# Performance work log

Measured on AMD Instinct MI355X. Metric: run time of the kernel, lower is better.

The kernel has to match this reference:

```python
import jax, jax.numpy as jnp
import numpy as np


def setup_inputs() -> dict:
    key = jax.random.key(0)
    k_x, k_w1, k_w2 = jax.random.split(key, 3)
    B, N, F, H = 32, 1024, 512, 2048
    x = jax.random.normal(k_x, (B, N, F), dtype=jnp.float32)
    # first: orthogonal-ish init (Gaussian is fine as a stand-in for correctness testing)
    W1 = jax.random.normal(k_w1, (H, F), dtype=jnp.float32) / np.sqrt(F)
    b1 = jnp.zeros((H,), dtype=jnp.float32)
    # second: normal(std=0.01)
    W2 = jax.random.normal(k_w2, (F, H), dtype=jnp.float32) * 0.01
    b2 = jnp.zeros((F,), dtype=jnp.float32)
    return {"x": x, "W1": W1, "b1": b1, "W2": W2, "b2": b2, "dim": 1}


def reference(x, W1, b1, W2, b2, dim):
    # Move the target feature axis (1 + dim) to last position.
    x = jnp.moveaxis(x, 1 + dim, -1)  # [B, N, F]
    srt = jnp.argsort(x, axis=-1)     # argsort indices
    inv = jnp.argsort(srt, axis=-1)   # inverse permutation
    # torch: x.scatter(-1, argsort, x) -> out[argsort[i]] = x[i] == gather by inverse
    xs = jnp.take_along_axis(x, inv, axis=-1)
    # 2-layer MLP with skip
    h = jax.nn.relu(jnp.einsum('bnf,hf->bnh', xs, W1) + b1)
    y = jnp.einsum('bnh,fh->bnf', h, W2) + b2 + xs
    # torch: y.scatter(-1, inverse, y) -> out[inverse[i]] = y[i] == gather by argsort
    out = jnp.take_along_axis(y, srt, axis=-1)
    return jnp.moveaxis(out, -1, 1 + dim)
```

## Files before the change

### kernel.cpp

```cpp
#include <hip/hip_runtime.h>
#include <hip/hip_bf16.h>

typedef __hip_bfloat16 bf16;
typedef __attribute__((ext_vector_type(8))) short bf16x8;
typedef __attribute__((ext_vector_type(4))) float f32x4;

#define ASYNC_CP16(gsrc, ldst)                                                              \
  __builtin_amdgcn_global_load_lds(                                                         \
      (const __attribute__((address_space(1))) unsigned int*)(gsrc),                        \
      (__attribute__((address_space(3))) unsigned int*)(ldst), 16, 0, 0)

#define BB 32
#define NN 1024
#define FF 512
#define HH 2048
#define M_ROWS (BB * NN)

__global__ __launch_bounds__(256) void cvt_pair(const float* __restrict__ a, bf16* __restrict__ da,
                                                const float* __restrict__ b, bf16* __restrict__ db,
                                                int n) {
  int i = blockIdx.x * 256 + threadIdx.x;
  if (i < n) {
    da[i] = __float2bfloat16(a[i]);
    db[i] = __float2bfloat16(b[i]);
  }
}

template <int CTRL>
__device__ __forceinline__ unsigned long long dpp_xor64(unsigned long long k) {
  int lo = (int)(unsigned)k;
  int hi = (int)(unsigned)(k >> 32);
  int plo = __builtin_amdgcn_update_dpp(lo, lo, CTRL, 0xF, 0xF, false);
  int phi = __builtin_amdgcn_update_dpp(hi, hi, CTRL, 0xF, 0xF, false);
  return (((unsigned long long)(unsigned)phi) << 32) | (unsigned)plo;
}

__global__ __launch_bounds__(256) void sort_rows_wave(const float* __restrict__ x,
                                                      unsigned* __restrict__ xs_pack,
                                                      unsigned* __restrict__ srt_pack) {
  __shared__ __align__(16) unsigned short scatx[4 * FF];
  const int t = threadIdx.x;
  const int lane = t & 63;
  const int w = t >> 6;
  const size_t row = (size_t)blockIdx.x * 4 + w;
  const float* xr = x + row * FF;

  float4 v0 = *(const float4*)(xr + lane * 8);
  float4 v1 = *(const float4*)(xr + lane * 8 + 4);
  float vals[8] = {v0.x, v0.y, v0.z, v0.w, v1.x, v1.y, v1.z, v1.w};

  unsigned long long key[8];
#pragma unroll
  for (int r = 0; r < 8; r++) {
    unsigned u = __float_as_uint(vals[r]);
    unsigned s = u ^ ((unsigned)((int)u >> 31) | 0x80000000u);
    key[r] = ((unsigned long long)s << 32) | (unsigned)(lane * 8 + r);
  }

#pragma unroll
  for (int k = 2; k <= 512; k <<= 1) {
#pragma unroll
    for (int j = k >> 1; j > 0; j >>= 1) {
      if (j >= 8) {
        const int d = j >> 3;
#pragma unroll
        for (int r = 0; r < 8; r++) {
          unsigned long long o;
          if (d == 1)       o = dpp_xor64<0xB1>(key[r]);
          else if (d == 2)  o = dpp_xor64<0x4E>(key[r]);
          else if (d == 8)  o = dpp_xor64<0x128>(key[r]);
          else              o = __shfl_xor(key[r], d, 64);
          bool asc = (((lane * 8 + r) & k) == 0);
          bool lower = ((lane & d) == 0);
          bool keepmin = (asc == lower);
          bool minemin = key[r] < o;
          key[r] = (minemin == keepmin) ? key[r] : o;
        }
      } else {
#pragma unroll
        for (int r = 0; r < 8; r++) {
          if ((r & j) == 0) {
            const int a = r, b = r | j;
            bool asc = (((lane * 8 + a) & k) == 0);
            unsigned long long ka = key[a], kb = key[b];
            bool sw = ((ka > kb) == asc);
            key[a] = sw ? kb : ka;
            key[b] = sw ? ka : kb;
          }
        }
      }
    }
  }

  const int base = w * FF;
  unsigned j8[8];
#pragma unroll
  for (int r = 0; r < 8; r++) {
    j8[r] = (unsigned)key[r] & 0xFFFFu;
    __hip_bfloat16 hb = __float2bfloat16(vals[r]);
    scatx[base + j8[r]] = *(unsigned short*)&hb;
  }

  uint4 so;
  so.x = j8[0] | (j8[1] << 16);
  so.y = j8[2] | (j8[3] << 16);
  so.z = j8[4] | (j8[5] << 16);
  so.w = j8[6] | (j8[7] << 16);
  *(uint4*)(srt_pack + row * 256 + lane * 4) = so;

  __syncthreads();
  uint4 xo = *(const uint4*)&scatx[base + lane * 8];
  *(uint4*)(xs_pack + row * 256 + lane * 4) = xo;
}

template <int RELU, int ADDX, int K, int N>
__global__ __launch_bounds__(512, 4) void gemm_fat(const bf16* __restrict__ A,
                                                   const bf16* __restrict__ Bw,
                                                   const float* __restrict__ bias,
                                                   const bf16* __restrict__ xs_add,
                                                   bf16* __restrict__ C) {
  __shared__ __align__(16) bf16 As[128 * 32];
  __shared__ __align__(16) bf16 Bs[256 * 32];
  const int t = threadIdx.x;
  const int lane = t & 63, wave = t >> 6;
  const int waveM = wave >> 2, waveN = wave & 3;
  const int srow = lane >> 2;
  const int scol = (lane & 3) * 8;
  const size_t mBase = (size_t)blockIdx.x * 128;
  const size_t nBase = (size_t)blockIdx.y * 256;
  const bf16* Ag  = A  + (mBase + wave * 16 + srow) * (size_t)K + scol;
  const bf16* Bg0 = Bw + (nBase + wave * 32 + srow) * (size_t)K + scol;
  const bf16* Bg1 = Bw + (nBase + wave * 32 + 16 + srow) * (size_t)K + scol;
  bf16* Al  = &As[wave * 16 * 32];
  bf16* Bl0 = &Bs[wave * 32 * 32];
  bf16* Bl1 = &Bs[(wave * 32 + 16) * 32];
  const int fr = lane & 15;
  const int fk = (lane >> 4) * 8;

  f32x4 acc[4][4];
  f32x4 zero = {0.f, 0.f, 0.f, 0.f};
#pragma unroll
  for (int i = 0; i < 4; i++)
#pragma unroll
    for (int j = 0; j < 4; j++) acc[i][j] = zero;

  for (int k0 = 0; k0 < K; k0 += 32) {
    ASYNC_CP16(Ag + k0, Al);
    ASYNC_CP16(Bg0 + k0, Bl0);
    ASYNC_CP16(Bg1 + k0, Bl1);
    __syncthreads();
    bf16x8 af[4], bfr[4];
#pragma unroll
    for (int mt = 0; mt < 4; mt++)
      af[mt] = *(const bf16x8*)&As[(waveM * 64 + mt * 16 + fr) * 32 + fk];
#pragma unroll
    for (int nt = 0; nt < 4; nt++)
      bfr[nt] = *(const bf16x8*)&Bs[(waveN * 64 + nt * 16 + fr) * 32 + fk];
#pragma unroll
    for (int mt = 0; mt < 4; mt++)
#pragma unroll
      for (int nt = 0; nt < 4; nt++)
        acc[mt][nt] = __builtin_amdgcn_mfma_f32_16x16x32_bf16(af[mt], bfr[nt], acc[mt][nt], 0, 0, 0);
    __syncthreads();
  }

  const int cn = lane & 15;
  const int cm = (lane >> 4) * 4;
  float b4[4];
#pragma unroll
  for (int nt = 0; nt < 4; nt++) b4[nt] = bias[nBase + waveN * 64 + nt * 16 + cn];
#pragma unroll
  for (int mt = 0; mt < 4; mt++) {
#pragma unroll
    for (int nt = 0; nt < 4; nt++) {
      size_t gn = nBase + waveN * 64 + nt * 16 + cn;
#pragma unroll
      for (int r = 0; r < 4; r++) {
        size_t gm = mBase + waveM * 64 + mt * 16 + cm + r;
        float v = acc[mt][nt][r] + b4[nt];
        if (RELU) v = fmaxf(v, 0.f);
        if (ADDX) v += __bfloat162float(xs_add[gm * N + gn]);
        C[gm * N + gn] = __float2bfloat16(v);
      }
    }
  }
}

__global__ __launch_bounds__(256) void permute_gather(const bf16* __restrict__ zp,
                                                      const unsigned* __restrict__ srt_pack,
                                                      float* __restrict__ out) {
  __shared__ __align__(16) unsigned short zr[4][FF];
  const int t = threadIdx.x;
  const int lane = t & 63;
  const int w = t >> 6;
  const size_t row = (size_t)blockIdx.x * 4 + w;

  *(uint4*)&zr[w][lane * 8] = *(const uint4*)(zp + row * FF + lane * 8);
  uint4 sv = *(const uint4*)(srt_pack + row * 256 + lane * 4);
  __syncthreads();

  unsigned idx[8] = {sv.x & 0xFFFFu, sv.x >> 16, sv.y & 0xFFFFu, sv.y >> 16,
                     sv.z & 0xFFFFu, sv.z >> 16, sv.w & 0xFFFFu, sv.w >> 16};
  float4 o0, o1;
#pragma unroll
  for (int r = 0; r < 8; r++) {
    float zf = __uint_as_float(((unsigned)zr[w][idx[r]]) << 16);
    ((r < 4) ? (&o0.x) : (&o1.x))[r & 3] = zf;
  }
  *(float4*)(out + row * FF + lane * 8) = o0;
  *(float4*)(out + row * FF + lane * 8 + 4) = o1;
}

extern "C" void kernel_launch(void* const* d_in, const int* in_sizes, int n_in,
                              void* d_out, int out_size, void* d_ws, size_t ws_size,
                              hipStream_t stream) {
  const float* x  = (const float*)d_in[0];
  const float* W1 = (const float*)d_in[1];
  const float* b1 = (const float*)d_in[2];
  const float* W2 = (const float*)d_in[3];
  const float* b2 = (const float*)d_in[4];
  float* out = (float*)d_out;

  char* ws = (char*)d_ws;
  unsigned* xs  = (unsigned*)(ws);
  bf16*     xsb = (bf16*)(ws);
  bf16*     z   = (bf16*)(ws);
  unsigned* srt = (unsigned*)(ws + 33554432);
  bf16* h   = (bf16*)(ws + 67108864);
  bf16* W1b = (bf16*)(ws + 201326592);
  bf16* W2b = (bf16*)(ws + 203423744);

  cvt_pair<<<(HH * FF + 255) / 256, 256, 0, stream>>>(W1, W1b, W2, W2b, HH * FF);
  sort_rows_wave<<<M_ROWS / 4, 256, 0, stream>>>(x, xs, srt);
  gemm_fat<1, 0, FF, HH><<<dim3(M_ROWS / 128, HH / 256), 512, 0, stream>>>(xsb, W1b, b1, nullptr, h);
  gemm_fat<0, 1, HH, FF><<<dim3(M_ROWS / 128, FF / 256), 512, 0, stream>>>(h, W2b, b2, xsb, z);
  permute_gather<<<M_ROWS / 4, 256, 0, stream>>>(z, srt, out);
}
```

Baseline: 376.0 us.

## Rewrite GEMM with 256x256 tiles, double-buffered LDS prefetch and swizzled layout

Replaces the single-buffered 128x256 GEMM with a 256x256 tile kernel. It stages the next 64-wide K slice into a second LDS buffer while MFMAs run on the current one, using XOR-swizzled LDS addressing to avoid bank conflicts. It also adds explicit waitcnt/barrier scheduling and setprio around the MFMA bursts. This aims to hide global-load latency and raise arithmetic intensity, at the cost of 128KB of LDS, 2 blocks per CU and more accumulator registers.

```diff
diff --git a/kernel.cpp b/kernel.cpp
--- a/kernel.cpp
+++ b/kernel.cpp
@@ -114,73 +114,161 @@
 }
 
 template <int RELU, int ADDX, int K, int N>
-__global__ __launch_bounds__(512, 4) void gemm_fat(const bf16* __restrict__ A,
-                                                   const bf16* __restrict__ Bw,
-                                                   const float* __restrict__ bias,
-                                                   const bf16* __restrict__ xs_add,
-                                                   bf16* __restrict__ C) {
-  __shared__ __align__(16) bf16 As[128 * 32];
-  __shared__ __align__(16) bf16 Bs[256 * 32];
+__global__ __launch_bounds__(512, 2) void gemm8p(const bf16* __restrict__ A,
+                                                 const bf16* __restrict__ Bw,
+                                                 const float* __restrict__ bias,
+                                                 const bf16* __restrict__ xs_add,
+                                                 bf16* __restrict__ C) {
+  __shared__ __align__(16) bf16 S[65536];
   const int t = threadIdx.x;
   const int lane = t & 63, wave = t >> 6;
   const int waveM = wave >> 2, waveN = wave & 3;
-  const int srow = lane >> 2;
-  const int scol = (lane & 3) * 8;
-  const size_t mBase = (size_t)blockIdx.x * 128;
+  const size_t mBase = (size_t)blockIdx.x * 256;
   const size_t nBase = (size_t)blockIdx.y * 256;
-  const bf16* Ag  = A  + (mBase + wave * 16 + srow) * (size_t)K + scol;
-  const bf16* Bg0 = Bw + (nBase + wave * 32 + srow) * (size_t)K + scol;
-  const bf16* Bg1 = Bw + (nBase + wave * 32 + 16 + srow) * (size_t)K + scol;
-  bf16* Al  = &As[wave * 16 * 32];
-  bf16* Bl0 = &Bs[wave * 32 * 32];
-  bf16* Bl1 = &Bs[(wave * 32 + 16) * 32];
+
+  const int srow = t >> 2;
+  const int sclog = (t & 3) ^ ((t >> 3) & 3);
+  const bf16* Asrc0 = A + (mBase + srow) * (size_t)K + sclog * 8;
+  const bf16* Bsrc0 = Bw + (nBase + srow) * (size_t)K + sclog * 8;
+  const int sdA = wave * 512;
+  const int sdB = 32768 + wave * 512;
+
   const int fr = lane & 15;
-  const int fk = (lane >> 4) * 8;
-
-  f32x4 acc[4][4];
+  const int swz8 = ((lane >> 4) ^ ((lane >> 1) & 3)) * 8;
+  const int aRd = (waveM * 128 + fr) * 32 + swz8;
+  const int bRd = 32768 + (waveN * 64 + fr) * 32 + swz8;
+
+#define STAGE_A(tt, ks)                                           \
+  do {                                                            \
+    const int rb_ = (((tt) & 1) * 2 + (ks)) * 8192 + sdA;         \
+    const bf16* g_ = Asrc0 + (size_t)(tt) * 64 + (ks) * 32;       \
+    ASYNC_CP16(g_, &S[rb_]);                                      \
+    ASYNC_CP16(g_ + (size_t)128 * K, &S[rb_ + 4096]);             \
+  } while (0)
+#define STAGE_B(tt, ks)                                           \
+  do {                                                            \
+    const int rb_ = (((tt) & 1) * 2 + (ks)) * 8192 + sdB;         \
+    const bf16* g_ = Bsrc0 + (size_t)(tt) * 64 + (ks) * 32;       \
+    ASYNC_CP16(g_, &S[rb_]);                                      \
+    ASYNC_CP16(g_ + (size_t)128 * K, &S[rb_ + 4096]);             \
+  } while (0)
+
+  f32x4 acc[8][4];
   f32x4 zero = {0.f, 0.f, 0.f, 0.f};
 #pragma unroll
-  for (int i = 0; i < 4; i++)
+  for (int i = 0; i < 8; i++)
 #pragma unroll
     for (int j = 0; j < 4; j++) acc[i][j] = zero;
 
-  for (int k0 = 0; k0 < K; k0 += 32) {
-    ASYNC_CP16(Ag + k0, Al);
-    ASYNC_CP16(Bg0 + k0, Bl0);
-    ASYNC_CP16(Bg1 + k0, Bl1);
-    __syncthreads();
-    bf16x8 af[4], bfr[4];
-#pragma unroll
-    for (int mt = 0; mt < 4; mt++)
-      af[mt] = *(const bf16x8*)&As[(waveM * 64 + mt * 16 + fr) * 32 + fk];
-#pragma unroll
-    for (int nt = 0; nt < 4; nt++)
-      bfr[nt] = *(const bf16x8*)&Bs[(waveN * 64 + nt * 16 + fr) * 32 + fk];
-#pragma unroll
-    for (int mt = 0; mt < 4; mt++)
-#pragma unroll
-      for (int nt = 0; nt < 4; nt++)
-        acc[mt][nt] = __builtin_amdgcn_mfma_f32_16x16x32_bf16(af[mt], bfr[nt], acc[mt][nt], 0, 0, 0);
-    __syncthreads();
-  }
+  STAGE_A(0, 0);
+  STAGE_B(0, 0);
+  STAGE_A(0, 1);
+  STAGE_B(0, 1);
+  asm volatile("s_waitcnt vmcnt(4)" ::: "memory");
+  __builtin_amdgcn_s_barrier();
+
+  const int NT = K / 64;
+  for (int kt = 0; kt < NT; ++kt) {
+    const int buf = kt & 1;
+    const bool pf = (kt + 1 < NT);
+    bf16x8 af[4], bq[4];
+
+    {
+      const int rg = buf * 16384;
+#pragma unroll
+      for (int i = 0; i < 4; i++) af[i] = *(const bf16x8*)&S[rg + aRd + i * 512];
+#pragma unroll
+      for (int n = 0; n < 4; n++) bq[n] = *(const bf16x8*)&S[rg + bRd + n * 512];
+      if (pf) STAGE_A(kt + 1, 0);
+      __builtin_amdgcn_s_barrier();
+      asm volatile("s_waitcnt lgkmcnt(0)" ::: "memory");
+      __builtin_amdgcn_sched_barrier(0);
+      __builtin_amdgcn_s_setprio(1);
+#pragma unroll
+      for (int i = 0; i < 4; i++)
+#pragma unroll
+        for (int n = 0; n < 4; n++)
+          acc[i][n] = __builtin_amdgcn_mfma_f32_16x16x32_bf16(af[i], bq[n], acc[i][n], 0, 0, 0);
+      __builtin_amdgcn_s_setprio(0);
+      __builtin_amdgcn_s_barrier();
+    }
+    {
+      const int rg = buf * 16384;
+#pragma unroll
+      for (int i = 0; i < 4; i++) af[i] = *(const bf16x8*)&S[rg + aRd + 2048 + i * 512];
+      if (pf) STAGE_B(kt + 1, 0);
+      __builtin_amdgcn_s_barrier();
+      asm volatile("s_waitcnt lgkmcnt(0)" ::: "memory");
+      __builtin_amdgcn_sched_barrier(0);
+      __builtin_amdgcn_s_setprio(1);
+#pragma unroll
+      for (int i = 0; i < 4; i++)
+#pragma unroll
+        for (int n = 0; n < 4; n++)
+          acc[4 + i][n] = __builtin_amdgcn_mfma_f32_16x16x32_bf16(af[i], bq[n], acc[4 + i][n], 0, 0, 0);
+      __builtin_amdgcn_s_setprio(0);
+      if (pf) asm volatile("s_waitcnt vmcnt(4)" ::: "memory");
+      else    asm volatile("s_waitcnt vmcnt(0)" ::: "memory");
+      __builtin_amdgcn_s_barrier();
+    }
+    {
+      const int rg = buf * 16384 + 8192;
+#pragma unroll
+      for (int i = 0; i < 4; i++) af[i] = *(const bf16x8*)&S[rg + aRd + i * 512];
+#pragma unroll
+      for (int n = 0; n < 4; n++) bq[n] = *(const bf16x8*)&S[rg + bRd + n * 512];
+      if (pf) STAGE_A(kt + 1, 1);
+      __builtin_amdgcn_s_barrier();
+      asm volatile("s_waitcnt lgkmcnt(0)" ::: "memory");
+      __builtin_amdgcn_sched_barrier(0);
+      __builtin_amdgcn_s_setprio(1);
+#pragma unroll
+      for (int i = 0; i < 4; i++)
+#pragma unroll
+        for (int n = 0; n < 4; n++)
+          acc[i][n] = __builtin_amdgcn_mfma_f32_16x16x32_bf16(af[i], bq[n], acc[i][n], 0, 0, 0);
+      __builtin_amdgcn_s_setprio(0);
+      __builtin_amdgcn_s_barrier();
+    }
+    {
+      const int rg = buf * 16384 + 8192;
+#pragma unroll
+      for (int i = 0; i < 4; i++) af[i] = *(const bf16x8*)&S[rg + aRd + 2048 + i * 512];
+      if (pf) STAGE_B(kt + 1, 1);
+      __builtin_amdgcn_s_barrier();
+      asm volatile("s_waitcnt lgkmcnt(0)" ::: "memory");
+      __builtin_amdgcn_sched_barrier(0);
+      __builtin_amdgcn_s_setprio(1);
+#pragma unroll
+      for (int i = 0; i < 4; i++)
+#pragma unroll
+        for (int n = 0; n < 4; n++)
+          acc[4 + i][n] = __builtin_amdgcn_mfma_f32_16x16x32_bf16(af[i], bq[n], acc[4 + i][n], 0, 0, 0);
+      __builtin_amdgcn_s_setprio(0);
+      if (pf) asm volatile("s_waitcnt vmcnt(4)" ::: "memory");
+      __builtin_amdgcn_s_barrier();
+    }
+  }
+#undef STAGE_A
+#undef STAGE_B
 
   const int cn = lane & 15;
   const int cm = (lane >> 4) * 4;
   float b4[4];
 #pragma unroll
-  for (int nt = 0; nt < 4; nt++) b4[nt] = bias[nBase + waveN * 64 + nt * 16 + cn];
-#pragma unroll
-  for (int mt = 0; mt < 4; mt++) {
-#pragma unroll
-    for (int nt = 0; nt < 4; nt++) {
-      size_t gn = nBase + waveN * 64 + nt * 16 + cn;
+  for (int n = 0; n < 4; n++) b4[n] = bias[nBase + waveN * 64 + n * 16 + cn];
+#pragma unroll
+  for (int mt = 0; mt < 8; mt++) {
+#pragma unroll
+    for (int n = 0; n < 4; n++) {
+      size_t gn = nBase + waveN * 64 + n * 16 + cn;
 #pragma unroll
       for (int r = 0; r < 4; r++) {
-        size_t gm = mBase + waveM * 64 + mt * 16 + cm + r;
-        float v = acc[mt][nt][r] + b4[nt];
+        size_t gm = mBase + waveM * 128 + mt * 16 + cm + r;
+        float v = acc[mt][n][r] + b4[n];
         if (RELU) v = fmaxf(v, 0.f);
-        if (ADDX) v += __bfloat162float(xs_add[gm * N + gn]);
-        C[gm * N + gn] = __float2bfloat16(v);
+        if (ADDX) v += __bfloat162float(xs_add[gm * (size_t)N + gn]);
+        C[gm * (size_t)N + gn] = __float2bfloat16(v);
       }
     }
   }
@@ -232,7 +320,7 @@
 
   cvt_pair<<<(HH * FF + 255) / 256, 256, 0, stream>>>(W1, W1b, W2, W2b, HH * FF);
   sort_rows_wave<<<M_ROWS / 4, 256, 0, stream>>>(x, xs, srt);
-  gemm_fat<1, 0, FF, HH><<<dim3(M_ROWS / 128, HH / 256), 512, 0, stream>>>(xsb, W1b, b1, nullptr, h);
-  gemm_fat<0, 1, HH, FF><<<dim3(M_ROWS / 128, FF / 256), 512, 0, stream>>>(h, W2b, b2, xsb, z);
+  gemm8p<1, 0, FF, HH><<<dim3(M_ROWS / 256, HH / 256), 512, 0, stream>>>(xsb, W1b, b1, nullptr, h);
+  gemm8p<0, 1, HH, FF><<<dim3(M_ROWS / 256, FF / 256), 512, 0, stream>>>(h, W2b, b2, xsb, z);
   permute_gather<<<M_ROWS / 4, 256, 0, stream>>>(z, srt, out);
 }
```

Result: faster. 356.0 us (-5.3%).
